# Kernel optimization log

Measured on AMD Instinct MI355X. Metric: run time of the kernel, lower is better.

## Reference

```python
import jax, jax.numpy as jnp
import numpy as np

B, S, D = 2, 2048, 2048
H, KV, HD = 32, 8, 64
REP = H // KV  # query heads per kv head
SCALE = np.float32(1.0 / np.sqrt(HD))


def setup_inputs() -> dict:
    key = jax.random.key(0)
    ks = jax.random.split(key, 5)
    x = jax.random.normal(ks[0], (B, S, D), dtype=jnp.float32)
    # RoPE tables: standard rotate_half convention, cos/sin shape [S, HD]
    inv_freq = 1.0 / (10000.0 ** (jnp.arange(0, HD, 2, dtype=jnp.float32) / HD))
    freqs = jnp.outer(jnp.arange(S, dtype=jnp.float32), inv_freq)  # [S, HD/2]
    emb = jnp.concatenate([freqs, freqs], axis=-1)  # [S, HD]
    cos, sin = jnp.cos(emb), jnp.sin(emb)
    std = np.float32(0.02)
    Wq = jax.random.normal(ks[1], (D, H * HD), dtype=jnp.float32) * std
    Wk = jax.random.normal(ks[2], (D, KV * HD), dtype=jnp.float32) * std
    Wv = jax.random.normal(ks[3], (D, KV * HD), dtype=jnp.float32) * std
    Wo = jax.random.normal(ks[4], (H * HD, D), dtype=jnp.float32) * std
    return {"x": x, "cos": cos, "sin": sin, "Wq": Wq, "Wk": Wk, "Wv": Wv, "Wo": Wo}


def _rotate_half(u):
    u1, u2 = jnp.split(u, 2, axis=-1)
    return jnp.concatenate([-u2, u1], axis=-1)


def reference(x, cos, sin, Wq, Wk, Wv, Wo):
    # projections -> [B, heads, S, HD]
    q = (x @ Wq).reshape(B, S, H, HD).transpose(0, 2, 1, 3)
    k = (x @ Wk).reshape(B, S, KV, HD).transpose(0, 2, 1, 3)
    v = (x @ Wv).reshape(B, S, KV, HD).transpose(0, 2, 1, 3)
    # RoPE on q and k (cos/sin broadcast over batch & head dims)
    c, s = cos[None, None], sin[None, None]
    q = q * c + _rotate_half(q) * s
    k = k * c + _rotate_half(k) * s
    # GQA: group query heads per kv head instead of materializing repeat_kv
    qg = q.reshape(B, KV, REP, S, HD)
    scores = jnp.einsum('bgrqd,bgkd->bgrqk', qg, k) * SCALE  # [B,KV,REP,S,S]
    causal = jnp.tril(jnp.ones((S, S), dtype=bool))
    scores = jnp.where(causal, scores, jnp.float32(-1e30))
    attn = jax.nn.softmax(scores, axis=-1)
    out = jnp.einsum('bgrqk,bgkd->bgrqd', attn, v)  # [B,KV,REP,S,HD]
    out = out.reshape(B, H, S, HD).transpose(0, 2, 1, 3).reshape(B, S, H * HD)
    return out @ Wo
```

## Files before the change

### kernel.cpp

```cpp
#include <hip/hip_runtime.h>

typedef unsigned short u16;
typedef __bf16 bfx8 __attribute__((ext_vector_type(8)));
typedef float f32x4 __attribute__((ext_vector_type(4)));
typedef float f32x16 __attribute__((ext_vector_type(16)));

#define MFMA16(a,b,c) __builtin_amdgcn_mfma_f32_16x16x32_bf16(a,b,c,0,0,0)
#define MFMA32(a,b,c) __builtin_amdgcn_mfma_f32_32x32x16_bf16(a,b,c,0,0,0)

__device__ __forceinline__ u16 f2bf(float f) {
  union { float f; unsigned u; } v; v.f = f;
  unsigned r = v.u + 0x7fffu + ((v.u >> 16) & 1u);
  return (u16)(r >> 16);
}

__device__ __forceinline__ unsigned cvtpk(float lo, float hi) {
  unsigned r;
  asm("v_cvt_pk_bf16_f32 %0, %1, %2" : "=v"(r) : "v"(lo), "v"(hi));
  return r;
}

__device__ __forceinline__ void swap32(unsigned &a, unsigned &b) {
  asm("v_permlane32_swap_b32 %0, %1" : "+v"(a), "+v"(b));
}

__device__ __forceinline__ void gld16(const void* g, void* l) {
  __builtin_amdgcn_global_load_lds(
      (const __attribute__((address_space(1))) unsigned int*)g,
      (__attribute__((address_space(3))) unsigned int*)l, 16, 0, 0);
}


__global__ void afrag_k(const float* __restrict__ in, u16* __restrict__ Af) {
  int i = blockIdx.x * 256 + threadIdx.x;
  int sm = i >> 8, d0 = (i & 255) * 8;
  const float* p = in + (size_t)sm * 2048 + d0;
  float4 a = *(const float4*)p;
  float4 b = *(const float4*)(p + 4);
  union { u16 h[8]; uint4 u; } o;
  o.h[0]=f2bf(a.x); o.h[1]=f2bf(a.y); o.h[2]=f2bf(a.z); o.h[3]=f2bf(a.w);
  o.h[4]=f2bf(b.x); o.h[5]=f2bf(b.y); o.h[6]=f2bf(b.z); o.h[7]=f2bf(b.w);
  int mt = sm >> 4, kt = d0 >> 5, lp = (sm & 15) + ((d0 >> 3) & 3) * 16;
  *(uint4*)(Af + ((size_t)(mt * 64 + kt) * 512 + lp * 8)) = o.u;
}

__global__ void bfrag_k(const float* __restrict__ W, u16* __restrict__ Bf,
                        int N, int ntoff) {
  __shared__ float tile[32][72];
  int nb = blockIdx.x, kb = blockIdx.y;
  int t = threadIdx.x;
  int r = t >> 3, c8 = (t & 7) * 8;
  const float* src = W + (size_t)(kb * 32 + r) * N + nb * 64 + c8;
  *(float4*)&tile[r][c8]     = *(const float4*)src;
  *(float4*)&tile[r][c8 + 4] = *(const float4*)(src + 4);
  __syncthreads();
  int fb = t >> 6, l = t & 63;
  int nn = fb * 16 + (l & 15), k0 = (l >> 4) * 8;
  union { u16 h[8]; uint4 u; } o;
  #pragma unroll
  for (int j = 0; j < 8; j++) o.h[j] = f2bf(tile[k0 + j][nn]);
  *(uint4*)(Bf + ((size_t)((ntoff + nb * 4 + fb) * 64 + kb) * 512 + l * 8)) = o.u;
}

__global__ __launch_bounds__(512, 4) void gemm_qkv(
    const u16* __restrict__ Af, const u16* __restrict__ Bf,
    const float* __restrict__ cosT, const float* __restrict__ sinT,
    u16* __restrict__ Qf, u16* __restrict__ Kf, u16* __restrict__ Vf) {
  __shared__ u16 lds[2 * 24 * 512];
  const int tid = threadIdx.x, lane = tid & 63, w = tid >> 6;
  const int wm = w >> 2, wn = w & 3;
  const int lrow = lane & 15, lg = lane >> 4;
  const int nwg = gridDim.x;
  const int per = nwg >> 3;
  const int swz = ((int)blockIdx.x & 7) * per + ((int)blockIdx.x >> 3);
  const int bm = swz / 12, bn = swz % 12;
  const int bm8 = bm * 8, bn16 = bn * 16;
  const int KT = 64;

  f32x4 acc[4][4] = {};
  u16* buf0 = lds;
  u16* buf1 = lds + 24 * 512;

  auto stageB = [&](int s, u16* dst) {
    #pragma unroll
    for (int j = 0; j < 2; j++) {
      int ng = w * 2 + j;
      gld16(Bf + ((size_t)(bn16 + ng) * KT + s) * 512 + lane * 8,
            dst + (8 + ng) * 512);
    }
  };
  auto stageA = [&](int s, u16* dst) {
    gld16(Af + ((size_t)(bm8 + w) * KT + s) * 512 + lane * 8,
          dst + w * 512);
  };

  stageB(0, buf0); stageA(0, buf0);
  stageB(1, buf1); stageA(1, buf1);
  asm volatile("s_waitcnt vmcnt(3)" ::: "memory");
  __builtin_amdgcn_s_barrier();

  bfx8 ar[2], br[4];
  for (int t = 0; t < KT; t++) {
    u16* rb = (t & 1) ? buf1 : buf0;
    const int s2 = (t + 2 < KT) ? t + 2 : 0;
    #pragma unroll
    for (int i = 0; i < 2; i++)
      ar[i] = *(const bfx8*)(rb + (wm * 4 + i) * 512 + lane * 8);
    #pragma unroll
    for (int j = 0; j < 4; j++)
      br[j] = *(const bfx8*)(rb + (8 + wn * 4 + j) * 512 + lane * 8);
    asm volatile("s_waitcnt lgkmcnt(0)" ::: "memory");
    __builtin_amdgcn_s_barrier();
    stageB(s2, rb);
    __builtin_amdgcn_s_setprio(1);
    #pragma unroll
    for (int i = 0; i < 2; i++)
      #pragma unroll
      for (int j = 0; j < 4; j++)
        acc[i][j] = MFMA16(ar[i], br[j], acc[i][j]);
    __builtin_amdgcn_s_setprio(0);
    __builtin_amdgcn_s_barrier();
    #pragma unroll
    for (int i = 0; i < 2; i++)
      ar[i] = *(const bfx8*)(rb + (wm * 4 + 2 + i) * 512 + lane * 8);
    asm volatile("s_waitcnt lgkmcnt(0)" ::: "memory");
    __builtin_amdgcn_s_barrier();
    stageA(s2, rb);
    __builtin_amdgcn_s_setprio(1);
    #pragma unroll
    for (int i = 0; i < 2; i++)
      #pragma unroll
      for (int j = 0; j < 4; j++)
        acc[2 + i][j] = MFMA16(ar[i], br[j], acc[2 + i][j]);
    __builtin_amdgcn_s_setprio(0);
    asm volatile("s_waitcnt vmcnt(3)" ::: "memory");
    __builtin_amdgcn_s_barrier();
  }
  asm volatile("s_waitcnt vmcnt(0)" ::: "memory");
  __builtin_amdgcn_s_barrier();

  const int hh = bn * 4 + wn;
  const int m0 = bm * 128 + wm * 64;
  u16* otw = lds + w * 2048;
  char* otb = (char*)otw;

  #pragma unroll
  for (int half = 0; half < 2; half++) {
    const int rowbase = m0 + half * 32;
    const int bb = rowbase >> 11;
    const int s0 = rowbase & 2047;
    if (hh < 40) {
      const float qsc = (hh < 32) ? 0.18033688f : 1.0f;
      #pragma unroll
      for (int mgl = 0; mgl < 2; mgl++) {
        const int mg = half * 2 + mgl;
        #pragma unroll
        for (int ng = 0; ng < 2; ng++) {
          const int d1 = ng * 16 + lrow;
          #pragma unroll
          for (int r = 0; r < 4; r++) {
            int s = s0 + mgl * 16 + lg * 4 + r;
            float a  = acc[mg][ng][r];
            float a2 = acc[mg][ng + 2][r];
            float c1 = cosT[s * 64 + d1],      s1v = sinT[s * 64 + d1];
            float c2 = cosT[s * 64 + d1 + 32], s2v = sinT[s * 64 + d1 + 32];
            float o1 = (a * c1 - a2 * s1v) * qsc;
            float o2 = (a2 * c2 + a * s2v) * qsc;
            int srow = mgl * 16 + lg * 4 + r;
            int swzb = (srow & 7) << 4;
            *(u16*)(otb + ((srow * 128 + d1 * 2) ^ swzb)) = f2bf(o1);
            *(u16*)(otb + ((srow * 128 + (d1 + 32) * 2) ^ swzb)) = f2bf(o2);
          }
        }
      }
      const int qt = s0 >> 5;
      u16* dst = (hh < 32)
          ? Qf + ((size_t)(bb * 32 + hh) * 64 + qt) * 2048
          : Kf + ((size_t)(bb * 8 + (hh - 32)) * 64 + qt) * 2048;
      const int srw = lane & 31;
      const int d0 = (lane >> 5) * 8;
      #pragma unroll
      for (int ks = 0; ks < 4; ks++) {
        int byte = ((srw * 128 + (ks * 16 + d0) * 2)) ^ ((srw & 7) << 4);
        uint4 v = *(uint4*)(otb + byte);
        *(uint4*)(dst + ks * 512 + lane * 8) = v;
      }
    } else {
      #pragma unroll
      for (int mgl = 0; mgl < 2; mgl++) {
        const int mg = half * 2 + mgl;
        #pragma unroll
        for (int ng = 0; ng < 4; ng++) {
          const int d = ng * 16 + lrow;
          #pragma unroll
          for (int r = 0; r < 4; r++) {
            int srow = mgl * 16 + lg * 4 + r;
            *(u16*)(otb + ((srow * 128 + d * 2) ^ ((srow & 7) << 4))) =
                f2bf(acc[mg][ng][r]);
          }
        }
      }
      const int kt = s0 >> 6;
      const int g = hh - 40;
      u16* dst = Vf + ((size_t)(bb * 8 + g) * 32 + kt) * 4096;
      const int d = lane & 31;
      const int hi8 = (lane >> 5) * 8;
      #pragma unroll
      for (int ks2 = 0; ks2 < 2; ks2++) {
        const int ks = half * 2 + ks2;
        #pragma unroll
        for (int sub = 0; sub < 2; sub++) {
          const int dd = sub * 32 + d;
          union { u16 h[8]; uint4 u; } o;
          #pragma unroll
          for (int j = 0; j < 8; j++) {
            int srow = ks2 * 16 + hi8 + j;
            o.h[j] = *(u16*)(otb + ((srow * 128 + dd * 2) ^ ((srow & 7) << 4)));
          }
          *(uint4*)(dst + (sub * 4 + ks) * 512 + lane * 8) = o.u;
        }
      }
    }
    __builtin_amdgcn_s_barrier();
  }
}

__global__ __launch_bounds__(512, 4) void gemm8p(
    const u16* __restrict__ Af, const u16* __restrict__ Bf,
    float* __restrict__ C, int N, int KT, int nbx) {
  __shared__ u16 lds[2 * 24 * 512];
  const int tid = threadIdx.x, lane = tid & 63, w = tid >> 6;
  const int wm = w >> 2, wn = w & 3;
  const int lrow = lane & 15, lg = lane >> 4;
  const int nwg = gridDim.x;
  const int per = nwg >> 3;
  const int swz = ((int)blockIdx.x & 7) * per + ((int)blockIdx.x >> 3);
  const int bm = swz / nbx, bn = swz % nbx;
  const int bm8 = bm * 8, bn16 = bn * 16;
  const int T = KT;

  f32x4 acc[4][4] = {};
  u16* buf0 = lds;
  u16* buf1 = lds + 24 * 512;

  auto stageB = [&](int s, u16* dst) {
    #pragma unroll
    for (int j = 0; j < 2; j++) {
      int ng = w * 2 + j;
      gld16(Bf + ((size_t)(bn16 + ng) * KT + s) * 512 + lane * 8,
            dst + (8 + ng) * 512);
    }
  };
  auto stageA = [&](int s, u16* dst) {
    gld16(Af + ((size_t)(bm8 + w) * KT + s) * 512 + lane * 8,
          dst + w * 512);
  };

  stageB(0, buf0); stageA(0, buf0);
  stageB(1, buf1); stageA(1, buf1);
  asm volatile("s_waitcnt vmcnt(3)" ::: "memory");
  __builtin_amdgcn_s_barrier();

  bfx8 ar[2], br[4];
  for (int t = 0; t < T; t++) {
    u16* rb = (t & 1) ? buf1 : buf0;
    const int s2 = (t + 2 < T) ? t + 2 : 0;
    #pragma unroll
    for (int i = 0; i < 2; i++)
      ar[i] = *(const bfx8*)(rb + (wm * 4 + i) * 512 + lane * 8);
    #pragma unroll
    for (int j = 0; j < 4; j++)
      br[j] = *(const bfx8*)(rb + (8 + wn * 4 + j) * 512 + lane * 8);
    asm volatile("s_waitcnt lgkmcnt(0)" ::: "memory");
    __builtin_amdgcn_s_barrier();
    stageB(s2, rb);
    __builtin_amdgcn_s_setprio(1);
    #pragma unroll
    for (int i = 0; i < 2; i++)
      #pragma unroll
      for (int j = 0; j < 4; j++)
        acc[i][j] = MFMA16(ar[i], br[j], acc[i][j]);
    __builtin_amdgcn_s_setprio(0);
    __builtin_amdgcn_s_barrier();
    #pragma unroll
    for (int i = 0; i < 2; i++)
      ar[i] = *(const bfx8*)(rb + (wm * 4 + 2 + i) * 512 + lane * 8);
    asm volatile("s_waitcnt lgkmcnt(0)" ::: "memory");
    __builtin_amdgcn_s_barrier();
    stageA(s2, rb);
    __builtin_amdgcn_s_setprio(1);
    #pragma unroll
    for (int i = 0; i < 2; i++)
      #pragma unroll
      for (int j = 0; j < 4; j++)
        acc[2 + i][j] = MFMA16(ar[i], br[j], acc[2 + i][j]);
    __builtin_amdgcn_s_setprio(0);
    asm volatile("s_waitcnt vmcnt(3)" ::: "memory");
    __builtin_amdgcn_s_barrier();
  }
  asm volatile("s_waitcnt vmcnt(0)" ::: "memory");

  const int m0 = bm * 128 + wm * 64, n0 = bn * 256 + wn * 64;
  #pragma unroll
  for (int mg = 0; mg < 4; mg++) {
    int row = m0 + mg * 16 + lg * 4;
    #pragma unroll
    for (int ng = 0; ng < 4; ng++) {
      int col = n0 + ng * 16 + lrow;
      float* cp = C + (size_t)row * N + col;
      #pragma unroll
      for (int r = 0; r < 4; r++) cp[(size_t)r * N] = acc[mg][ng][r];
    }
  }
}

__global__ __launch_bounds__(256, 2) void attn_k(
    const u16* __restrict__ Qf, const u16* __restrict__ Kf,
    const u16* __restrict__ Vf, u16* __restrict__ Aof)
{
  __shared__ u16 ot[4][32 * 64];
  const int tid = threadIdx.x, lane = tid & 63, w = tid >> 6;
  const int h = blockIdx.y, b = blockIdx.z;
  const int kvh = h >> 2;
  const int ql = lane & 31, hi = lane >> 5;
  const int qrA = blockIdx.x * 4 + w;

  const u16* Qh = Qf + (size_t)(b * 32 + h) * 131072;
  const u16* Kp = Kf + (size_t)(b * 8 + kvh) * 131072;
  const u16* Vp = Vf + (size_t)(b * 8 + kvh) * 131072;

  #pragma unroll
  for (int half = 0; half < 2; half++) {
    const int qr = half ? qrA : 63 - qrA;
    const int q0 = qr * 32;
    const int qg = q0 + ql;
    const int nkt = qr / 2 + 1;

    bfx8 qf[4];
    #pragma unroll
    for (int ks = 0; ks < 4; ks++)
      qf[ks] = *(const bfx8*)(Qh + (size_t)qr * 2048 + ks * 512 + lane * 8);

    f32x16 oacc0 = {}, oacc1 = {};
    float m2 = -3.0e38f;
    float lsum = 0.f;

    bfx8 ka[8];
    #pragma unroll
    for (int i = 0; i < 8; i++)
      ka[i] = *(const bfx8*)(Kp + i * 512 + lane * 8);

    for (int kt = 0; kt < nkt; kt++) {
      const int kb = kt * 64;
      bfx8 va[8];
      #pragma unroll
      for (int i = 0; i < 8; i++)
        va[i] = *(const bfx8*)(Vp + (size_t)kt * 4096 + i * 512 + lane * 8);
      f32x16 st0 = {}, st1 = {};
      #pragma unroll
      for (int ks = 0; ks < 4; ks++) {
        st0 = MFMA32(ka[ks], qf[ks], st0);
        st1 = MFMA32(ka[4 + ks], qf[ks], st1);
      }
      const int ktn = (kt + 1 < nkt) ? kt + 1 : 0;
      bfx8 kn[8];
      #pragma unroll
      for (int i = 0; i < 8; i++)
        kn[i] = *(const bfx8*)(Kp + (size_t)ktn * 4096 + i * 512 + lane * 8);
      if (kt == nkt - 1) {
        #pragma unroll
        for (int r = 0; r < 16; r++) {
          int crow = (r & 3) + 8 * (r >> 2) + 4 * hi;
          if (kb + crow > qg) st0[r] = -3.0e38f;
          if (kb + 32 + crow > qg) st1[r] = -3.0e38f;
        }
      }
      float mx[16];
      #pragma unroll
      for (int r = 0; r < 16; r++) mx[r] = fmaxf(st0[r], st1[r]);
      #pragma unroll
      for (int s = 8; s > 0; s >>= 1)
        #pragma unroll
        for (int r = 0; r < s; r++) mx[r] = fmaxf(mx[r], mx[r + s]);
      float tm = fmaxf(mx[0], __shfl_xor(mx[0], 32));
      float mnew = fmaxf(m2, tm);
      if (!__all(tm <= m2 + 8.0f)) {
        float corr = exp2f(m2 - mnew);
        lsum *= corr;
        #pragma unroll
        for (int i = 0; i < 16; i++) { oacc0[i] *= corr; oacc1[i] *= corr; }
        m2 = mnew;
      }
      #pragma unroll
      for (int r = 0; r < 16; r++) { st0[r] = exp2f(st0[r] - m2); }
      #pragma unroll
      for (int r = 0; r < 16; r++) { st1[r] = exp2f(st1[r] - m2); }
      float sm[16];
      #pragma unroll
      for (int r = 0; r < 16; r++) sm[r] = st0[r] + st1[r];
      #pragma unroll
      for (int s = 8; s > 0; s >>= 1)
        #pragma unroll
        for (int r = 0; r < s; r++) sm[r] += sm[r + s];
      lsum += sm[0];
      bfx8 pb[4];
      #pragma unroll
      for (int ks = 0; ks < 4; ks++) {
        int o = (ks & 1) * 8;
        unsigned X = cvtpk(ks < 2 ? st0[o + 0] : st1[o + 0], ks < 2 ? st0[o + 1] : st1[o + 1]);
        unsigned Z = cvtpk(ks < 2 ? st0[o + 2] : st1[o + 2], ks < 2 ? st0[o + 3] : st1[o + 3]);
        unsigned Y = cvtpk(ks < 2 ? st0[o + 4] : st1[o + 4], ks < 2 ? st0[o + 5] : st1[o + 5]);
        unsigned W = cvtpk(ks < 2 ? st0[o + 6] : st1[o + 6], ks < 2 ? st0[o + 7] : st1[o + 7]);
        swap32(X, Y);
        swap32(Z, W);
        union { unsigned u[4]; bfx8 v; } uu;
        uu.u[0] = X; uu.u[1] = Z; uu.u[2] = Y; uu.u[3] = W;
        pb[ks] = uu.v;
      }
      #pragma unroll
      for (int ks = 0; ks < 4; ks++) {
        oacc0 = MFMA32(va[ks], pb[ks], oacc0);
        oacc1 = MFMA32(va[4 + ks], pb[ks], oacc1);
      }
      #pragma unroll
      for (int i = 0; i < 8; i++) ka[i] = kn[i];
    }
    lsum += __shfl_xor(lsum, 32);
    float inv = 1.f / lsum;
    u16* my = ot[w];
    #pragma unroll
    for (int dt = 0; dt < 2; dt++) {
      #pragma unroll
      for (int g = 0; g < 4; g++) {
        float a0 = (dt ? oacc1[g*4+0] : oacc0[g*4+0]) * inv;
        float a1 = (dt ? oacc1[g*4+1] : oacc0[g*4+1]) * inv;
        float a2 = (dt ? oacc1[g*4+2] : oacc0[g*4+2]) * inv;
        float a3 = (dt ? oacc1[g*4+3] : oacc0[g*4+3]) * inv;
        unsigned w0 = cvtpk(a0, a1), w1 = cvtpk(a2, a3);
        int d = dt * 32 + g * 8 + 4 * hi;
        int byte = (ql * 128 + d * 2) ^ ((ql & 7) << 4);
        *(uint2*)((char*)my + byte) = make_uint2(w0, w1);
      }
    }
    #pragma unroll
    for (int rr = 0; rr < 4; rr++) {
      int q = rr * 8 + (lane >> 3);
      int dk = (lane & 7) * 8;
      int byte = (q * 128 + dk * 2) ^ ((q & 7) << 4);
      uint4 val = *(uint4*)((char*)my + byte);
      int mt = b * 128 + qr * 2 + (q >> 4);
      int ktg = h * 2 + (dk >> 5);
      int lp = (q & 15) + ((dk >> 3) & 3) * 16;
      *(uint4*)(Aof + ((size_t)(mt * 64 + ktg) * 512 + lp * 8)) = val;
    }
  }
}

extern "C" void kernel_launch(void* const* d_in, const int* in_sizes, int n_in,
                              void* d_out, int out_size, void* d_ws, size_t ws_size,
                              hipStream_t stream) {
  const float* x    = (const float*)d_in[0];
  const float* cosT = (const float*)d_in[1];
  const float* sinT = (const float*)d_in[2];
  const float* Wq   = (const float*)d_in[3];
  const float* Wk   = (const float*)d_in[4];
  const float* Wv   = (const float*)d_in[5];
  const float* Wo   = (const float*)d_in[6];
  float* out = (float*)d_out;
  char* ws = (char*)d_ws;

  u16* Af   = (u16*)(ws);
  u16* Bqkv = (u16*)(ws + 16777216);
  u16* Bwo  = (u16*)(ws + 29360128);
  u16* Qf   = (u16*)(ws + 37748736);
  u16* Kf   = (u16*)(ws + 54525952);
  u16* Vf   = (u16*)(ws + 58720256);
  u16* Aof  = (u16*)(ws + 62914560);

  afrag_k<<<4096, 256, 0, stream>>>(x, Af);
  bfrag_k<<<dim3(32, 64), 256, 0, stream>>>(Wq, Bqkv, 2048, 0);
  bfrag_k<<<dim3(8, 64), 256, 0, stream>>>(Wk, Bqkv, 512, 128);
  bfrag_k<<<dim3(8, 64), 256, 0, stream>>>(Wv, Bqkv, 512, 160);
  bfrag_k<<<dim3(32, 64), 256, 0, stream>>>(Wo, Bwo, 2048, 0);

  gemm_qkv<<<384, 512, 0, stream>>>(Af, Bqkv, cosT, sinT, Qf, Kf, Vf);

  attn_k<<<dim3(8, 32, 2), 256, 0, stream>>>(Qf, Kf, Vf, Aof);

  gemm8p<<<256, 512, 0, stream>>>(Aof, Bwo, out, 2048, 64, 8);
}
```

Before: 200.8 us.

## Split attention KV range across wave pairs and merge partial softmax in LDS

Each block now handles one balanced pair of query row-tiles, and two waves share each row-tile by splitting its KV tiles in half (split-K flash attention). The partial max, sum and output accumulators are merged through shared memory after a barrier. The grid grows fourfold and launch bounds rise to 3 blocks per CU, shortening the per-wave serial KV loop to expose more parallelism. In exchange, the K prefetch into the next iteration is dropped, LDS use and a sync are added, and only half the waves write output.

```diff
diff --git a/kernel.cpp b/kernel.cpp
--- a/kernel.cpp
+++ b/kernel.cpp
@@ -314,120 +314,134 @@
   }
 }
 
-__global__ __launch_bounds__(256, 2) void attn_k(
+__global__ __launch_bounds__(256, 3) void attn_k(
     const u16* __restrict__ Qf, const u16* __restrict__ Kf,
     const u16* __restrict__ Vf, u16* __restrict__ Aof)
 {
-  __shared__ u16 ot[4][32 * 64];
+  __shared__ float mO[2][32 * 64];
+  __shared__ float mm[2][64], ml[2][64];
+  __shared__ u16 ot[2][32 * 64];
   const int tid = threadIdx.x, lane = tid & 63, w = tid >> 6;
   const int h = blockIdx.y, b = blockIdx.z;
   const int kvh = h >> 2;
   const int ql = lane & 31, hi = lane >> 5;
-  const int qrA = blockIdx.x * 4 + w;
+  const int qrA = blockIdx.x;
+  const int pr = w >> 1, sub = w & 1;
+  const int qr = pr ? qrA : 63 - qrA;
+  const int q0 = qr * 32;
+  const int qg = q0 + ql;
+  const int nkt = qr / 2 + 1;
+  const int hf = (nkt + 1) >> 1;
+  const int tbeg = sub ? hf : 0;
+  const int tend = sub ? nkt : hf;
 
   const u16* Qh = Qf + (size_t)(b * 32 + h) * 131072;
   const u16* Kp = Kf + (size_t)(b * 8 + kvh) * 131072;
   const u16* Vp = Vf + (size_t)(b * 8 + kvh) * 131072;
 
+  bfx8 qf[4];
   #pragma unroll
-  for (int half = 0; half < 2; half++) {
-    const int qr = half ? qrA : 63 - qrA;
-    const int q0 = qr * 32;
-    const int qg = q0 + ql;
-    const int nkt = qr / 2 + 1;
-
-    bfx8 qf[4];
-    #pragma unroll
-    for (int ks = 0; ks < 4; ks++)
-      qf[ks] = *(const bfx8*)(Qh + (size_t)qr * 2048 + ks * 512 + lane * 8);
-
-    f32x16 oacc0 = {}, oacc1 = {};
-    float m2 = -3.0e38f;
-    float lsum = 0.f;
-
+  for (int ks = 0; ks < 4; ks++)
+    qf[ks] = *(const bfx8*)(Qh + (size_t)qr * 2048 + ks * 512 + lane * 8);
+
+  f32x16 oacc0 = {}, oacc1 = {};
+  float m2 = -3.0e38f;
+  float lsum = 0.f;
+
+  for (int kt = tbeg; kt < tend; kt++) {
+    const int kb = kt * 64;
     bfx8 ka[8];
     #pragma unroll
     for (int i = 0; i < 8; i++)
-      ka[i] = *(const bfx8*)(Kp + i * 512 + lane * 8);
-
-    for (int kt = 0; kt < nkt; kt++) {
-      const int kb = kt * 64;
-      bfx8 va[8];
-      #pragma unroll
-      for (int i = 0; i < 8; i++)
-        va[i] = *(const bfx8*)(Vp + (size_t)kt * 4096 + i * 512 + lane * 8);
-      f32x16 st0 = {}, st1 = {};
-      #pragma unroll
-      for (int ks = 0; ks < 4; ks++) {
-        st0 = MFMA32(ka[ks], qf[ks], st0);
-        st1 = MFMA32(ka[4 + ks], qf[ks], st1);
+      ka[i] = *(const bfx8*)(Kp + (size_t)kt * 4096 + i * 512 + lane * 8);
+    bfx8 va[8];
+    #pragma unroll
+    for (int i = 0; i < 8; i++)
+      va[i] = *(const bfx8*)(Vp + (size_t)kt * 4096 + i * 512 + lane * 8);
+    f32x16 st0 = {}, st1 = {};
+    #pragma unroll
+    for (int ks = 0; ks < 4; ks++) {
+      st0 = MFMA32(ka[ks], qf[ks], st0);
+      st1 = MFMA32(ka[4 + ks], qf[ks], st1);
+    }
+    if (kt == nkt - 1) {
+      #pragma unroll
+      for (int r = 0; r < 16; r++) {
+        int crow = (r & 3) + 8 * (r >> 2) + 4 * hi;
+        if (kb + crow > qg) st0[r] = -3.0e38f;
+        if (kb + 32 + crow > qg) st1[r] = -3.0e38f;
       }
-      const int ktn = (kt + 1 < nkt) ? kt + 1 : 0;
-      bfx8 kn[8];
-      #pragma unroll
-      for (int i = 0; i < 8; i++)
-        kn[i] = *(const bfx8*)(Kp + (size_t)ktn * 4096 + i * 512 + lane * 8);
-      if (kt == nkt - 1) {
-        #pragma unroll
-        for (int r = 0; r < 16; r++) {
-          int crow = (r & 3) + 8 * (r >> 2) + 4 * hi;
-          if (kb + crow > qg) st0[r] = -3.0e38f;
-          if (kb + 32 + crow > qg) st1[r] = -3.0e38f;
-        }
-      }
-      float mx[16];
-      #pragma unroll
-      for (int r = 0; r < 16; r++) mx[r] = fmaxf(st0[r], st1[r]);
-      #pragma unroll
-      for (int s = 8; s > 0; s >>= 1)
-        #pragma unroll
-        for (int r = 0; r < s; r++) mx[r] = fmaxf(mx[r], mx[r + s]);
-      float tm = fmaxf(mx[0], __shfl_xor(mx[0], 32));
-      float mnew = fmaxf(m2, tm);
-      if (!__all(tm <= m2 + 8.0f)) {
-        float corr = exp2f(m2 - mnew);
-        lsum *= corr;
-        #pragma unroll
-        for (int i = 0; i < 16; i++) { oacc0[i] *= corr; oacc1[i] *= corr; }
-        m2 = mnew;
-      }
-      #pragma unroll
-      for (int r = 0; r < 16; r++) { st0[r] = exp2f(st0[r] - m2); }
-      #pragma unroll
-      for (int r = 0; r < 16; r++) { st1[r] = exp2f(st1[r] - m2); }
-      float sm[16];
-      #pragma unroll
-      for (int r = 0; r < 16; r++) sm[r] = st0[r] + st1[r];
-      #pragma unroll
-      for (int s = 8; s > 0; s >>= 1)
-        #pragma unroll
-        for (int r = 0; r < s; r++) sm[r] += sm[r + s];
-      lsum += sm[0];
-      bfx8 pb[4];
-      #pragma unroll
-      for (int ks = 0; ks < 4; ks++) {
-        int o = (ks & 1) * 8;
-        unsigned X = cvtpk(ks < 2 ? st0[o + 0] : st1[o + 0], ks < 2 ? st0[o + 1] : st1[o + 1]);
-        unsigned Z = cvtpk(ks < 2 ? st0[o + 2] : st1[o + 2], ks < 2 ? st0[o + 3] : st1[o + 3]);
-        unsigned Y = cvtpk(ks < 2 ? st0[o + 4] : st1[o + 4], ks < 2 ? st0[o + 5] : st1[o + 5]);
-        unsigned W = cvtpk(ks < 2 ? st0[o + 6] : st1[o + 6], ks < 2 ? st0[o + 7] : st1[o + 7]);
-        swap32(X, Y);
-        swap32(Z, W);
-        union { unsigned u[4]; bfx8 v; } uu;
-        uu.u[0] = X; uu.u[1] = Z; uu.u[2] = Y; uu.u[3] = W;
-        pb[ks] = uu.v;
-      }
-      #pragma unroll
-      for (int ks = 0; ks < 4; ks++) {
-        oacc0 = MFMA32(va[ks], pb[ks], oacc0);
-        oacc1 = MFMA32(va[4 + ks], pb[ks], oacc1);
-      }
-      #pragma unroll
-      for (int i = 0; i < 8; i++) ka[i] = kn[i];
-    }
+    }
+    float mx[16];
+    #pragma unroll
+    for (int r = 0; r < 16; r++) mx[r] = fmaxf(st0[r], st1[r]);
+    #pragma unroll
+    for (int s = 8; s > 0; s >>= 1)
+      #pragma unroll
+      for (int r = 0; r < s; r++) mx[r] = fmaxf(mx[r], mx[r + s]);
+    float tm = fmaxf(mx[0], __shfl_xor(mx[0], 32));
+    float mnew = fmaxf(m2, tm);
+    if (!__all(tm <= m2 + 8.0f)) {
+      float corr = exp2f(m2 - mnew);
+      lsum *= corr;
+      #pragma unroll
+      for (int i = 0; i < 16; i++) { oacc0[i] *= corr; oacc1[i] *= corr; }
+      m2 = mnew;
+    }
+    #pragma unroll
+    for (int r = 0; r < 16; r++) { st0[r] = exp2f(st0[r] - m2); }
+    #pragma unroll
+    for (int r = 0; r < 16; r++) { st1[r] = exp2f(st1[r] - m2); }
+    float sm[16];
+    #pragma unroll
+    for (int r = 0; r < 16; r++) sm[r] = st0[r] + st1[r];
+    #pragma unroll
+    for (int s = 8; s > 0; s >>= 1)
+      #pragma unroll
+      for (int r = 0; r < s; r++) sm[r] += sm[r + s];
+    lsum += sm[0];
+    bfx8 pb[4];
+    #pragma unroll
+    for (int ks = 0; ks < 4; ks++) {
+      int o = (ks & 1) * 8;
+      unsigned X = cvtpk(ks < 2 ? st0[o + 0] : st1[o + 0], ks < 2 ? st0[o + 1] : st1[o + 1]);
+      unsigned Z = cvtpk(ks < 2 ? st0[o + 2] : st1[o + 2], ks < 2 ? st0[o + 3] : st1[o + 3]);
+      unsigned Y = cvtpk(ks < 2 ? st0[o + 4] : st1[o + 4], ks < 2 ? st0[o + 5] : st1[o + 5]);
+      unsigned W = cvtpk(ks < 2 ? st0[o + 6] : st1[o + 6], ks < 2 ? st0[o + 7] : st1[o + 7]);
+      swap32(X, Y);
+      swap32(Z, W);
+      union { unsigned u[4]; bfx8 v; } uu;
+      uu.u[0] = X; uu.u[1] = Z; uu.u[2] = Y; uu.u[3] = W;
+      pb[ks] = uu.v;
+    }
+    #pragma unroll
+    for (int ks = 0; ks < 4; ks++) {
+      oacc0 = MFMA32(va[ks], pb[ks], oacc0);
+      oacc1 = MFMA32(va[4 + ks], pb[ks], oacc1);
+    }
+  }
+
+  if (sub) {
+    #pragma unroll
+    for (int i = 0; i < 16; i++) mO[pr][i * 64 + lane] = oacc0[i];
+    #pragma unroll
+    for (int i = 0; i < 16; i++) mO[pr][(16 + i) * 64 + lane] = oacc1[i];
+    mm[pr][lane] = m2;
+    ml[pr][lane] = lsum;
+  }
+  __syncthreads();
+  if (!sub) {
+    float mB = mm[pr][lane], lB = ml[pr][lane];
+    float mn = fmaxf(m2, mB);
+    float cA = exp2f(m2 - mn), cB = exp2f(mB - mn);
+    lsum = lsum * cA + lB * cB;
+    #pragma unroll
+    for (int i = 0; i < 16; i++) oacc0[i] = oacc0[i] * cA + mO[pr][i * 64 + lane] * cB;
+    #pragma unroll
+    for (int i = 0; i < 16; i++) oacc1[i] = oacc1[i] * cA + mO[pr][(16 + i) * 64 + lane] * cB;
     lsum += __shfl_xor(lsum, 32);
     float inv = 1.f / lsum;
-    u16* my = ot[w];
+    u16* my = ot[pr];
     #pragma unroll
     for (int dt = 0; dt < 2; dt++) {
       #pragma unroll
@@ -485,7 +499,7 @@
 
   gemm_qkv<<<384, 512, 0, stream>>>(Af, Bqkv, cosT, sinT, Qf, Kf, Vf);
 
-  attn_k<<<dim3(8, 32, 2), 256, 0, stream>>>(Qf, Kf, Vf, Aof);
+  attn_k<<<dim3(32, 32, 2), 256, 0, stream>>>(Qf, Kf, Vf, Aof);
 
   gemm8p<<<256, 512, 0, stream>>>(Aof, Bwo, out, 2048, 64, 8);
 }
```

Result: slower. 227.1 us (+13.1%).
